# Optimization experiments

Measured on AMD Instinct MI355X. Metric: run time of the kernel, lower is better.

The kernel has to match this reference:

```python
import jax, jax.numpy as jnp
import numpy as np

N_NODES = 100000
N_EDGES = 1600000
IN_DIM = 128
OUT_DIM = 128


def setup_inputs() -> dict:
    key = jax.random.key(0)
    k1, k2, k3, k4, k5 = jax.random.split(key, 5)
    x = jax.random.normal(k1, (N_NODES, IN_DIM), dtype=jnp.float32)
    edge_index = jax.random.randint(k2, (2, N_EDGES), 0, N_NODES, dtype=jnp.int64)
    s = 1.0 / np.sqrt(IN_DIM)
    # PyG SAGEConv params: lin_l (neighbor branch, with bias), lin_r (root branch, no bias)
    W_l = jax.random.uniform(k3, (OUT_DIM, IN_DIM), jnp.float32, -s, s)
    b_l = jax.random.uniform(k4, (OUT_DIM,), jnp.float32, -s, s)
    W_r = jax.random.uniform(k5, (OUT_DIM, IN_DIM), jnp.float32, -s, s)
    return {"x": x, "edge_index": edge_index, "W_l": W_l, "b_l": b_l, "W_r": W_r}


def reference(x, edge_index, W_l, b_l, W_r):
    src = edge_index[0]  # message source j
    dst = edge_index[1]  # aggregation target i
    # mean aggregation of neighbor features at each target node
    msg_sum = jax.ops.segment_sum(x[src], dst, num_segments=N_NODES)  # [N, in]
    deg = jax.ops.segment_sum(jnp.ones((N_EDGES,), x.dtype), dst, num_segments=N_NODES)
    agg = msg_sum / jnp.maximum(deg, 1.0)[:, None]
    # out = lin_l(agg) + lin_r(x)
    out = agg @ W_l.T + b_l + x @ W_r.T  # [N, out]
    # L2 normalize (F.normalize, p=2, dim=-1, eps=1e-12)
    norm = jnp.sqrt(jnp.sum(out * out, axis=-1, keepdims=True))
    out = out / jnp.maximum(norm, 1e-12)
    return out
```

## Files before the change

kernel.cpp:

```cpp
#include <hip/hip_runtime.h>
#include <hip/hip_fp16.h>
#include <stdint.h>

#define NN 100000
#define D 128
#define W0 128
#define NB ((NN + W0 - 1) / W0)
#define C1 4096

typedef _Float16 f16x8 __attribute__((ext_vector_type(8)));
typedef float f32x4 __attribute__((ext_vector_type(4)));

static const size_t O_FLAG   = 0;
static const size_t O_BCNT   = 256;
static const size_t O_BSTART = O_BCNT + 4096;
static const size_t O_BCUR   = O_BSTART + 4096;
static const size_t O_WTL    = O_BCUR + 4096;
static const size_t O_WTR    = O_WTL + (size_t)D * D * 4;
static const size_t O_OFFS   = O_WTR + (size_t)D * D * 4;
static const size_t O_DEG    = O_OFFS + (size_t)(NN + 64) * 4;
static const size_t O_RECS   = O_DEG + (size_t)NN * 4;

__global__ void k_detect(const int* __restrict__ ei, int* flag, long long E) {
    int l = threadIdx.x;
    int bad = 0;
    if (l < E)       bad |= (ei[2 * l + 1] != 0);
    if (l + 64 < E)  bad |= (ei[2 * (l + 64) + 1] != 0);
    unsigned long long m = __ballot(bad);
    if (l == 0) *flag = (m == 0ull) ? 1 : 0;
}

__device__ __forceinline__ int edge_at(const int* ei, long long pos, int is64) {
    return is64 ? ei[2 * pos] : ei[pos];
}

__global__ void k_transpose(const float* __restrict__ Wl, const float* __restrict__ Wr,
                            float* __restrict__ WtL, float* __restrict__ WtR) {
    int t = blockIdx.x * 256 + threadIdx.x;
    if (t < D * D) {
        int o = t >> 7, k = t & 127;
        WtL[k * D + o] = Wl[t];
        WtR[k * D + o] = Wr[t];
    }
}

__global__ __launch_bounds__(256) void k_pack(const float* __restrict__ Wl,
                                              const float* __restrict__ Wr,
                                              __half* __restrict__ Bp) {
    int idx = blockIdx.x * 256 + threadIdx.x;
    if (idx >= 32768) return;
    int j  = idx & 7;
    int l  = (idx >> 3) & 63;
    int tt = (idx >> 9) & 7;
    int s  = idx >> 12;
    int col = tt * 16 + (l & 15);
    int k   = s * 32 + (l >> 4) * 8 + j;
    float v = (k < 128) ? Wl[col * 128 + k] : Wr[col * 128 + (k - 128)];
    Bp[idx] = __float2half_rn(v);
}

__global__ __launch_bounds__(256) void k_conv(const float* __restrict__ x,
                                              __half* __restrict__ xh, long long n4) {
    long long i = (long long)blockIdx.x * 256 + threadIdx.x;
    if (i >= n4) return;
    float4 v = ((const float4*)x)[i];
    __half2 h0 = __floats2half2_rn(v.x, v.y);
    __half2 h1 = __floats2half2_rn(v.z, v.w);
    ((__half2*)xh)[2 * i]     = h0;
    ((__half2*)xh)[2 * i + 1] = h1;
}

__global__ __launch_bounds__(256) void k_p1count(const int* __restrict__ ei,
                                                 const int* __restrict__ flag,
                                                 int* __restrict__ bcount,
                                                 int* __restrict__ bhist, long long E) {
    __shared__ int cnt[NB];
    for (int i = threadIdx.x; i < NB; i += 256) cnt[i] = 0;
    __syncthreads();
    int is64 = *flag;
    long long base = (long long)blockIdx.x * C1;
    for (int j = threadIdx.x; j < C1; j += 256) {
        long long e = base + j;
        if (e < E) {
            int d = edge_at(ei, E + e, is64);
            atomicAdd(&cnt[d >> 7], 1);
        }
    }
    __syncthreads();
    for (int i = threadIdx.x; i < NB; i += 256) {
        int c = cnt[i];
        if (bhist) bhist[(long long)blockIdx.x * NB + i] = c;
        if (c) atomicAdd(&bcount[i], c);
    }
}

__global__ __launch_bounds__(1024) void k_bscan(const int* __restrict__ bcount,
                                                int* __restrict__ bstart,
                                                int* __restrict__ bcur,
                                                int* __restrict__ offs) {
    __shared__ int sh[1024];
    int t = threadIdx.x;
    sh[t] = (t < NB) ? bcount[t] : 0;
    __syncthreads();
    for (int d = 1; d < 1024; d <<= 1) {
        int v = (t >= d) ? sh[t - d] : 0;
        __syncthreads();
        sh[t] += v;
        __syncthreads();
    }
    if (t < NB) {
        int ex = (t > 0) ? sh[t - 1] : 0;
        bstart[t] = ex;
        bcur[t] = ex;
    }
    if (t == NB - 1) {
        bstart[NB] = sh[NB - 1];
        offs[NN] = sh[NB - 1];
    }
}

__global__ __launch_bounds__(256) void k_p1scatter2(const int* __restrict__ ei,
                                                    const int* __restrict__ flag,
                                                    int* __restrict__ bcur,
                                                    const int* __restrict__ bhist,
                                                    unsigned int* __restrict__ recs,
                                                    long long E) {
    __shared__ int cnt[NB];
    __shared__ int rbase[NB];
    int t = threadIdx.x;
    const int* h = bhist + (long long)blockIdx.x * NB;
    for (int i = t; i < NB; i += 256) {
        int c = h[i];
        rbase[i] = c ? atomicAdd(&bcur[i], c) : 0;
        cnt[i] = 0;
    }
    __syncthreads();
    int is64 = *flag;
    long long base = (long long)blockIdx.x * C1;
    for (int j = t; j < C1; j += 256) {
        long long e = base + j;
        if (e < E) {
            int s = edge_at(ei, e, is64);
            int d = edge_at(ei, E + e, is64);
            int bu = d >> 7;
            int pos = rbase[bu] + atomicAdd(&cnt[bu], 1);
            recs[pos] = (unsigned)s | ((unsigned)(d & (W0 - 1)) << 20);
        }
    }
}

__global__ __launch_bounds__(256) void k_p1scatter(const int* __restrict__ ei,
                                                   const int* __restrict__ flag,
                                                   int* __restrict__ bcur,
                                                   unsigned int* __restrict__ recs,
                                                   long long E) {
    __shared__ int cnt[NB];
    __shared__ int rbase[NB];
    for (int i = threadIdx.x; i < NB; i += 256) cnt[i] = 0;
    __syncthreads();
    int is64 = *flag;
    long long base = (long long)blockIdx.x * C1;
    for (int j = threadIdx.x; j < C1; j += 256) {
        long long e = base + j;
        if (e < E) {
            int d = edge_at(ei, E + e, is64);
            atomicAdd(&cnt[d >> 7], 1);
        }
    }
    __syncthreads();
    for (int i = threadIdx.x; i < NB; i += 256) {
        int c = cnt[i];
        rbase[i] = c ? atomicAdd(&bcur[i], c) : 0;
    }
    __syncthreads();
    for (int i = threadIdx.x; i < NB; i += 256) cnt[i] = 0;
    __syncthreads();
    for (int j = threadIdx.x; j < C1; j += 256) {
        long long e = base + j;
        if (e < E) {
            int s = edge_at(ei, e, is64);
            int d = edge_at(ei, E + e, is64);
            int bu = d >> 7;
            int pos = rbase[bu] + atomicAdd(&cnt[bu], 1);
            recs[pos] = (unsigned)s | ((unsigned)(d & (W0 - 1)) << 20);
        }
    }
}

__global__ __launch_bounds__(256) void k_p2(const unsigned int* __restrict__ recs,
                                            const int* __restrict__ bstart,
                                            int* __restrict__ offs,
                                            int* __restrict__ srcs, int N) {
    __shared__ int cnt[W0];
    __shared__ int off[W0];
    int t = threadIdx.x;
    int bu = blockIdx.x;
    int e0 = bstart[bu], e1 = bstart[bu + 1];
    if (t < W0) cnt[t] = 0;
    __syncthreads();
    for (int e = e0 + t; e < e1; e += 256)
        atomicAdd(&cnt[recs[e] >> 20], 1);
    __syncthreads();
    if (t < W0) off[t] = cnt[t];
    __syncthreads();
    for (int d = 1; d < W0; d <<= 1) {
        int v = 0;
        if (t < W0 && t >= d) v = off[t - d];
        __syncthreads();
        if (t < W0) off[t] += v;
        __syncthreads();
    }
    if (t < W0) {
        int ex = (t > 0) ? off[t - 1] : 0;
        int node = bu * W0 + t;
        if (node < N) offs[node] = e0 + ex;
        cnt[t] = e0 + ex;
    }
    __syncthreads();
    for (int e = e0 + t; e < e1; e += 256) {
        unsigned r = recs[e];
        int pos = atomicAdd(&cnt[r >> 20], 1);
        srcs[pos] = (int)(r & 0xFFFFFu);
    }
}

__global__ __launch_bounds__(256) void k_agg_hh4(const __half* __restrict__ xh,
                                                 const int* __restrict__ offs,
                                                 const int* __restrict__ srcs,
                                                 __half* __restrict__ agg, int N) {
    int lane = threadIdx.x & 63;
    int wid  = __builtin_amdgcn_readfirstlane(threadIdx.x >> 6);
    int node = blockIdx.x * 4 + wid;
    if (node >= N) return;
    int e0 = offs[node], e1 = offs[node + 1];
    int grp = lane >> 4;
    int li  = lane & 15;
    float acc[8] = {0.f, 0.f, 0.f, 0.f, 0.f, 0.f, 0.f, 0.f};
    for (int e = e0; e < e1; e += 4) {
        int ee = e + grp;
        bool ok = ee < e1;
        int s = srcs[ok ? ee : e0];
        f16x8 v = *(const f16x8*)(xh + (long long)s * 128 + li * 8);
        if (ok) {
#pragma unroll
            for (int j = 0; j < 8; ++j) acc[j] += (float)v[j];
        }
    }
#pragma unroll
    for (int j = 0; j < 8; ++j) {
        acc[j] += __shfl_xor(acc[j], 16, 64);
        acc[j] += __shfl_xor(acc[j], 32, 64);
    }
    if (grp == 0) {
        float inv = 1.0f / fmaxf((float)(e1 - e0), 1.0f);
        __half2 o[4];
#pragma unroll
        for (int j = 0; j < 4; ++j)
            o[j] = __floats2half2_rn(acc[2 * j] * inv, acc[2 * j + 1] * inv);
        *(float4*)(agg + (long long)node * 128 + li * 8) = *(float4*)o;
    }
}

__global__ __launch_bounds__(256) void k_agg_h(const __half* __restrict__ xh,
                                               const int* __restrict__ offs,
                                               const int* __restrict__ srcs,
                                               float* agg, int N) {
    int lane = threadIdx.x & 63;
    int wid = __builtin_amdgcn_readfirstlane(threadIdx.x >> 6);
    int node = blockIdx.x * 4 + wid;
    if (node >= N) return;
    int e0 = offs[node], e1 = offs[node + 1];
    const __half2* x2 = (const __half2*)xh;
    float ax = 0.f, ay = 0.f;
    int e = e0;
    for (; e + 4 <= e1; e += 4) {
        int s0 = srcs[e], s1 = srcs[e + 1], s2 = srcs[e + 2], s3 = srcs[e + 3];
        float2 v0 = __half22float2(x2[(long long)s0 * 64 + lane]);
        float2 v1 = __half22float2(x2[(long long)s1 * 64 + lane]);
        float2 v2 = __half22float2(x2[(long long)s2 * 64 + lane]);
        float2 v3 = __half22float2(x2[(long long)s3 * 64 + lane]);
        ax += v0.x + v1.x + v2.x + v3.x;
        ay += v0.y + v1.y + v2.y + v3.y;
    }
    for (; e < e1; ++e) {
        int s = srcs[e];
        float2 v = __half22float2(x2[(long long)s * 64 + lane]);
        ax += v.x; ay += v.y;
    }
    float inv = 1.0f / fmaxf((float)(e1 - e0), 1.0f);
    float2 o; o.x = ax * inv; o.y = ay * inv;
    ((float2*)agg)[(long long)node * 64 + lane] = o;
}

__global__ __launch_bounds__(256) void k_agg(const float* __restrict__ x,
                                             const int* __restrict__ offs,
                                             const int* __restrict__ srcs,
                                             float* agg, int N) {
    int lane = threadIdx.x & 63;
    int wid = __builtin_amdgcn_readfirstlane(threadIdx.x >> 6);
    int node = blockIdx.x * 4 + wid;
    if (node >= N) return;
    int e0 = offs[node], e1 = offs[node + 1];
    const float2* x2 = (const float2*)x;
    float ax = 0.f, ay = 0.f;
    int e = e0;
    for (; e + 4 <= e1; e += 4) {
        int s0 = srcs[e], s1 = srcs[e + 1], s2 = srcs[e + 2], s3 = srcs[e + 3];
        float2 v0 = x2[(long long)s0 * 64 + lane];
        float2 v1 = x2[(long long)s1 * 64 + lane];
        float2 v2 = x2[(long long)s2 * 64 + lane];
        float2 v3 = x2[(long long)s3 * 64 + lane];
        ax += v0.x + v1.x + v2.x + v3.x;
        ay += v0.y + v1.y + v2.y + v3.y;
    }
    for (; e < e1; ++e) {
        int s = srcs[e];
        float2 v = x2[(long long)s * 64 + lane];
        ax += v.x; ay += v.y;
    }
    float inv = 1.0f / fmaxf((float)(e1 - e0), 1.0f);
    float2 o; o.x = ax * inv; o.y = ay * inv;
    ((float2*)agg)[(long long)node * 64 + lane] = o;
}

__global__ __launch_bounds__(256) void k_scatterB(const float* __restrict__ x,
                                                  const int* __restrict__ ei,
                                                  const int* __restrict__ flag,
                                                  float* out, float* deg, long long E) {
    int lane = threadIdx.x & 63;
    long long e = (long long)blockIdx.x * 4 + (threadIdx.x >> 6);
    if (e >= E) return;
    int is64 = *flag;
    int s = edge_at(ei, e, is64);
    int d = edge_at(ei, E + e, is64);
    atomicAdd(&out[(long long)d * D + lane], x[(long long)s * D + lane]);
    atomicAdd(&out[(long long)d * D + 64 + lane], x[(long long)s * D + 64 + lane]);
    if (lane == 0) atomicAdd(&deg[d], 1.0f);
}

__global__ void k_meanB(float* out, const float* __restrict__ deg) {
    long long i = (long long)blockIdx.x * 256 + threadIdx.x;
    if (i >= (long long)NN * D) return;
    out[i] *= 1.0f / fmaxf(deg[i >> 7], 1.0f);
}

__global__ __launch_bounds__(256) void k_gemm_m(const __half* __restrict__ aggh,
                                                const __half* __restrict__ xh,
                                                const __half* __restrict__ Bp,
                                                const float* __restrict__ bl,
                                                float* __restrict__ out, int N) {
    __shared__ __half Bs[32768];
    int t = threadIdx.x;
#pragma unroll
    for (int i = 0; i < 16; ++i) {
        int idx = t + i * 256;
        ((float4*)Bs)[idx] = ((const float4*)Bp)[idx];
    }
    int lane = t & 63;
    int wid  = t >> 6;
    int row0 = blockIdx.x * 128 + wid * 32;
    int rA = row0 + (lane & 15);
    int rB = rA + 16;
    long long ra = (rA < N) ? rA : (N - 1);
    long long rb = (rB < N) ? rB : (N - 1);
    int koff = (lane >> 4) * 8;

    f32x4 acc[2][8];
#pragma unroll
    for (int r = 0; r < 2; ++r)
#pragma unroll
        for (int c = 0; c < 8; ++c)
            acc[r][c] = (f32x4){0.f, 0.f, 0.f, 0.f};

    __syncthreads();

#pragma unroll
    for (int s = 0; s < 8; ++s) {
        const __half* Ap = (s < 4) ? aggh : xh;
        int kb = (s & 3) * 32 + koff;
        f16x8 a0 = *(const f16x8*)(Ap + ra * 128 + kb);
        f16x8 a1 = *(const f16x8*)(Ap + rb * 128 + kb);
        const __half* bs = Bs + s * 4096 + lane * 8;
#pragma unroll
        for (int tt = 0; tt < 8; ++tt) {
            f16x8 b = *(const f16x8*)(bs + tt * 512);
            acc[0][tt] = __builtin_amdgcn_mfma_f32_16x16x32_f16(a0, b, acc[0][tt], 0, 0, 0);
            acc[1][tt] = __builtin_amdgcn_mfma_f32_16x16x32_f16(a1, b, acc[1][tt], 0, 0, 0);
        }
    }

    float bias[8];
#pragma unroll
    for (int tt = 0; tt < 8; ++tt) bias[tt] = bl[tt * 16 + (lane & 15)];

#pragma unroll
    for (int rt = 0; rt < 2; ++rt) {
#pragma unroll
        for (int r = 0; r < 4; ++r) {
            int row = row0 + rt * 16 + (lane >> 4) * 4 + r;
            float v[8];
            float ss = 0.f;
#pragma unroll
            for (int tt = 0; tt < 8; ++tt) {
                v[tt] = acc[rt][tt][r] + bias[tt];
                ss = fmaf(v[tt], v[tt], ss);
            }
            ss += __shfl_xor(ss, 1, 64);
            ss += __shfl_xor(ss, 2, 64);
            ss += __shfl_xor(ss, 4, 64);
            ss += __shfl_xor(ss, 8, 64);
            float scale = 1.0f / fmaxf(sqrtf(ss), 1e-12f);
            if (row < N) {
                float* op = out + (long long)row * D + (lane & 15);
#pragma unroll
                for (int tt = 0; tt < 8; ++tt)
                    op[tt * 16] = v[tt] * scale;
            }
        }
    }
}

__global__ __launch_bounds__(256) void k_gemm(const float* __restrict__ x,
                                              const float* agg,
                                              const float* __restrict__ WtL,
                                              const float* __restrict__ WtR,
                                              const float* __restrict__ bl,
                                              float* out, int N) {
    __shared__ float Bs[64 * D];
    int t = threadIdx.x;
    int tx = t & 15;
    int ty = t >> 4;
    int row0 = blockIdx.x * 64 + ty * 4;
    int c0a = tx * 4;
    int c0b = 64 + tx * 4;

    float acc[4][8];
    float4 b0 = *(const float4*)(bl + c0a);
    float4 b1 = *(const float4*)(bl + c0b);
#pragma unroll
    for (int r = 0; r < 4; ++r) {
        acc[r][0] = b0.x; acc[r][1] = b0.y; acc[r][2] = b0.z; acc[r][3] = b0.w;
        acc[r][4] = b1.x; acc[r][5] = b1.y; acc[r][6] = b1.z; acc[r][7] = b1.w;
    }

    long long rws[4];
#pragma unroll
    for (int r = 0; r < 4; ++r) {
        int rr = row0 + r;
        rws[r] = (rr < N) ? (long long)rr : (long long)(N - 1);
    }

    for (int phase = 0; phase < 2; ++phase) {
        const float* A = phase ? x : agg;
        const float* W = phase ? WtR : WtL;
        const float4* Ar0 = (const float4*)(A + rws[0] * D);
        const float4* Ar1 = (const float4*)(A + rws[1] * D);
        const float4* Ar2 = (const float4*)(A + rws[2] * D);
        const float4* Ar3 = (const float4*)(A + rws[3] * D);

        for (int half = 0; half < 2; ++half) {
            if (phase | half) __syncthreads();
#pragma unroll
            for (int i = 0; i < 8; ++i) {
                int idx = t + i * 256;
                ((float4*)Bs)[idx] = ((const float4*)(W + half * 64 * D))[idx];
            }
            __syncthreads();

#pragma unroll 2
            for (int k4 = 0; k4 < 16; ++k4) {
                int ak4 = half * 16 + k4;
                float4 av[4];
                av[0] = Ar0[ak4]; av[1] = Ar1[ak4]; av[2] = Ar2[ak4]; av[3] = Ar3[ak4];
#pragma unroll
                for (int kk = 0; kk < 4; ++kk) {
                    int k = k4 * 4 + kk;
                    float4 w0 = *(const float4*)&Bs[k * D + c0a];
                    float4 w1 = *(const float4*)&Bs[k * D + c0b];
#pragma unroll
                    for (int r = 0; r < 4; ++r) {
                        float a = (kk == 0) ? av[r].x : (kk == 1) ? av[r].y
                                 : (kk == 2) ? av[r].z : av[r].w;
                        acc[r][0] = fmaf(a, w0.x, acc[r][0]);
                        acc[r][1] = fmaf(a, w0.y, acc[r][1]);
                        acc[r][2] = fmaf(a, w0.z, acc[r][2]);
                        acc[r][3] = fmaf(a, w0.w, acc[r][3]);
                        acc[r][4] = fmaf(a, w1.x, acc[r][4]);
                        acc[r][5] = fmaf(a, w1.y, acc[r][5]);
                        acc[r][6] = fmaf(a, w1.z, acc[r][6]);
                        acc[r][7] = fmaf(a, w1.w, acc[r][7]);
                    }
                }
            }
        }
    }

#pragma unroll
    for (int r = 0; r < 4; ++r) {
        float s = 0.f;
#pragma unroll
        for (int j = 0; j < 8; ++j) s = fmaf(acc[r][j], acc[r][j], s);
        s += __shfl_xor(s, 1, 64);
        s += __shfl_xor(s, 2, 64);
        s += __shfl_xor(s, 4, 64);
        s += __shfl_xor(s, 8, 64);
        float scale = 1.0f / fmaxf(sqrtf(s), 1e-12f);
        int rr = row0 + r;
        if (rr < N) {
            float4 v0, v1;
            v0.x = acc[r][0] * scale; v0.y = acc[r][1] * scale;
            v0.z = acc[r][2] * scale; v0.w = acc[r][3] * scale;
            v1.x = acc[r][4] * scale; v1.y = acc[r][5] * scale;
            v1.z = acc[r][6] * scale; v1.w = acc[r][7] * scale;
            float* op = out + (long long)rr * D;
            *(float4*)(op + c0a) = v0;
            *(float4*)(op + c0b) = v1;
        }
    }
}

extern "C" void kernel_launch(void* const* d_in, const int* in_sizes, int n_in,
                              void* d_out, int out_size, void* d_ws, size_t ws_size,
                              hipStream_t stream) {
    const float* x  = (const float*)d_in[0];
    const int*   ei = (const int*)d_in[1];
    const float* Wl = (const float*)d_in[2];
    const float* bl = (const float*)d_in[3];
    const float* Wr = (const float*)d_in[4];
    float* out = (float*)d_out;
    const long long E = (long long)in_sizes[1] / 2;

    char* ws = (char*)d_ws;
    int*      flag   = (int*)(ws + O_FLAG);
    int*      bcount = (int*)(ws + O_BCNT);
    int*      bstart = (int*)(ws + O_BSTART);
    int*      bcur   = (int*)(ws + O_BCUR);
    float*    WtL    = (float*)(ws + O_WTL);
    float*    WtR    = (float*)(ws + O_WTR);
    __half*   Bph    = (__half*)(ws + O_WTL);
    int*      offs   = (int*)(ws + O_OFFS);
    float*    deg    = (float*)(ws + O_DEG);
    unsigned* recs   = (unsigned*)(ws + O_RECS);
    int*      srcs   = (int*)(ws + O_RECS + (size_t)E * 4);
    const size_t O_XH = O_RECS + (size_t)E * 8;
    __half*   xh     = (__half*)(ws + O_XH);
    const size_t O_AGGH = O_XH + (size_t)NN * D * 2;
    __half*   aggh   = (__half*)(ws + O_AGGH);
    const size_t O_BHIST = O_AGGH + (size_t)NN * D * 2;
    int*      bhist  = (int*)(ws + O_BHIST);

    int pblocks = (int)((E + C1 - 1) / C1);
    size_t planA_bytes  = O_RECS + (size_t)E * 8;
    size_t fp16_bytes   = O_XH + (size_t)NN * D * 2;
    size_t mfma_bytes   = O_AGGH + (size_t)NN * D * 2;
    size_t merged_bytes = O_BHIST + (size_t)pblocks * NB * 4;
    bool planA    = ws_size >= planA_bytes;
    bool useH     = ws_size >= fp16_bytes;
    bool useM     = planA && (ws_size >= mfma_bytes);
    bool useMerge = useM && (ws_size >= merged_bytes);

    k_detect<<<1, 64, 0, stream>>>(ei, flag, E);
    if (useM)
        k_pack<<<128, 256, 0, stream>>>(Wl, Wr, Bph);
    else
        k_transpose<<<(D * D + 255) / 256, 256, 0, stream>>>(Wl, Wr, WtL, WtR);

    if (planA) {
        hipMemsetAsync(ws + O_BCNT, 0, (size_t)NB * 4, stream);
        if (useH) {
            long long n4 = (long long)NN * D / 4;
            k_conv<<<(int)((n4 + 255) / 256), 256, 0, stream>>>(x, xh, n4);
        }
        k_p1count<<<pblocks, 256, 0, stream>>>(ei, flag, bcount,
                                               useMerge ? bhist : (int*)nullptr, E);
        k_bscan<<<1, 1024, 0, stream>>>(bcount, bstart, bcur, offs);
        if (useMerge)
            k_p1scatter2<<<pblocks, 256, 0, stream>>>(ei, flag, bcur, bhist, recs, E);
        else
            k_p1scatter<<<pblocks, 256, 0, stream>>>(ei, flag, bcur, recs, E);
        k_p2<<<NB, 256, 0, stream>>>(recs, bstart, offs, srcs, NN);
        if (useM) {
            k_agg_hh4<<<(NN + 3) / 4, 256, 0, stream>>>(xh, offs, srcs, aggh, NN);
            k_gemm_m<<<(NN + 127) / 128, 256, 0, stream>>>(aggh, xh, Bph, bl, out, NN);
            return;
        }
        if (useH)
            k_agg_h<<<(NN + 3) / 4, 256, 0, stream>>>(xh, offs, srcs, out, NN);
        else
            k_agg<<<(NN + 3) / 4, 256, 0, stream>>>(x, offs, srcs, out, NN);
    } else {
        hipMemsetAsync(out, 0, (size_t)NN * D * 4, stream);
        hipMemsetAsync(ws + O_DEG, 0, (size_t)NN * 4, stream);
        k_scatterB<<<(int)((E + 3) / 4), 256, 0, stream>>>(x, ei, flag, out, deg, E);
        k_meanB<<<(int)(((long long)NN * D + 255) / 256), 256, 0, stream>>>(out, deg);
    }
    k_gemm<<<(NN + 63) / 64, 256, 0, stream>>>(x, out, WtL, WtR, bl, out, NN);
}
```

Measured before the change: 266.7 us.

## Split aggregation across feature slices with per-block node chunks

Replaces the one-wave-per-node fp16 gather with a kernel where each block handles one 16-column feature slice for a 256-node chunk. Eight blocks cover the eight slices. Within a wave, 4 nodes × 8 edges × 2 halves are processed at once, and partial sums are reduced by shuffles. The intent is to narrow the working set touched per block so the gathered rows get better cache locality. In exchange each source row is fetched in 32-byte pieces by eight separate blocks and the srcs/offs reads are repeated eight times.

```diff
diff --git a/kernel.cpp b/kernel.cpp
--- a/kernel.cpp
+++ b/kernel.cpp
@@ -224,40 +224,47 @@
     }
 }
 
-__global__ __launch_bounds__(256) void k_agg_hh4(const __half* __restrict__ xh,
-                                                 const int* __restrict__ offs,
-                                                 const int* __restrict__ srcs,
-                                                 __half* __restrict__ agg, int N) {
-    int lane = threadIdx.x & 63;
-    int wid  = __builtin_amdgcn_readfirstlane(threadIdx.x >> 6);
-    int node = blockIdx.x * 4 + wid;
-    if (node >= N) return;
-    int e0 = offs[node], e1 = offs[node + 1];
-    int grp = lane >> 4;
-    int li  = lane & 15;
-    float acc[8] = {0.f, 0.f, 0.f, 0.f, 0.f, 0.f, 0.f, 0.f};
-    for (int e = e0; e < e1; e += 4) {
-        int ee = e + grp;
-        bool ok = ee < e1;
-        int s = srcs[ok ? ee : e0];
-        f16x8 v = *(const f16x8*)(xh + (long long)s * 128 + li * 8);
-        if (ok) {
-#pragma unroll
-            for (int j = 0; j < 8; ++j) acc[j] += (float)v[j];
-        }
-    }
-#pragma unroll
-    for (int j = 0; j < 8; ++j) {
-        acc[j] += __shfl_xor(acc[j], 16, 64);
-        acc[j] += __shfl_xor(acc[j], 32, 64);
-    }
-    if (grp == 0) {
-        float inv = 1.0f / fmaxf((float)(e1 - e0), 1.0f);
-        __half2 o[4];
-#pragma unroll
-        for (int j = 0; j < 4; ++j)
-            o[j] = __floats2half2_rn(acc[2 * j] * inv, acc[2 * j + 1] * inv);
-        *(float4*)(agg + (long long)node * 128 + li * 8) = *(float4*)o;
+__global__ __launch_bounds__(256) void k_agg_s(const __half* __restrict__ xh,
+                                               const int* __restrict__ offs,
+                                               const int* __restrict__ srcs,
+                                               __half* __restrict__ agg, int N) {
+    int slice = blockIdx.x & 7;
+    int chunk = blockIdx.x >> 3;
+    int lane  = threadIdx.x & 63;
+    int wid   = __builtin_amdgcn_readfirstlane(threadIdx.x >> 6);
+    int n_in  = lane >> 4;
+    int e_in  = (lane >> 1) & 7;
+    int h     = lane & 1;
+    int dbase = slice * 16 + h * 8;
+
+    for (int r = 0; r < 16; ++r) {
+        int node = chunk * 256 + r * 16 + wid * 4 + n_in;
+        if (node >= N) return;
+        int e0 = offs[node], e1 = offs[node + 1];
+        float acc[8] = {0.f, 0.f, 0.f, 0.f, 0.f, 0.f, 0.f, 0.f};
+        for (int e = e0; e < e1; e += 8) {
+            int ee = e + e_in;
+            if (ee < e1) {
+                int s = srcs[ee];
+                f16x8 v = *(const f16x8*)(xh + (long long)s * 128 + dbase);
+#pragma unroll
+                for (int j = 0; j < 8; ++j) acc[j] += (float)v[j];
+            }
+        }
+#pragma unroll
+        for (int j = 0; j < 8; ++j) {
+            acc[j] += __shfl_xor(acc[j], 2, 64);
+            acc[j] += __shfl_xor(acc[j], 4, 64);
+            acc[j] += __shfl_xor(acc[j], 8, 64);
+        }
+        if (e_in == 0) {
+            float inv = 1.0f / fmaxf((float)(e1 - e0), 1.0f);
+            __half2 o[4];
+#pragma unroll
+            for (int j = 0; j < 4; ++j)
+                o[j] = __floats2half2_rn(acc[2 * j] * inv, acc[2 * j + 1] * inv);
+            *(float4*)(agg + (long long)node * 128 + dbase) = *(float4*)o;
+        }
     }
 }
 
@@ -580,7 +587,8 @@
             k_p1scatter<<<pblocks, 256, 0, stream>>>(ei, flag, bcur, recs, E);
         k_p2<<<NB, 256, 0, stream>>>(recs, bstart, offs, srcs, NN);
         if (useM) {
-            k_agg_hh4<<<(NN + 3) / 4, 256, 0, stream>>>(xh, offs, srcs, aggh, NN);
+            int nchunk = (NN + 255) / 256;
+            k_agg_s<<<8 * nchunk, 256, 0, stream>>>(xh, offs, srcs, aggh, NN);
             k_gemm_m<<<(NN + 127) / 128, 256, 0, stream>>>(aggh, xh, Bph, bl, out, NN);
             return;
         }
```

Result: slower. 387.7 us (+45.4%).

## Fuse CSR preprocessing into one cooperative kernel with grid syncs

Applied to the files above, without the earlier changes.

Replaces the chain of detect, pack, convert, count, scan, scatter and per-bucket sort kernels with a single cooperative kernel of NB blocks that uses grid.sync between phases, removing several launches and the memset. Each block now loops over multiple edge chunks and keeps its histogram in shared memory across the grid barrier, so the per-chunk global bhist buffer is no longer needed. The aggregation kernel is swapped back to a half2-per-lane variant with 8-way unrolled gathers. Risks include cooperative-launch occupancy limits for 782 blocks with large shared arrays, fewer blocks doing the edge pass, and grid-barrier cost.

```diff
diff --git a/kernel.cpp b/kernel.cpp
--- a/kernel.cpp
+++ b/kernel.cpp
@@ -1,6 +1,9 @@
 #include <hip/hip_runtime.h>
 #include <hip/hip_fp16.h>
+#include <hip/hip_cooperative_groups.h>
 #include <stdint.h>
+
+namespace cg = cooperative_groups;
 
 #define NN 100000
 #define D 128
@@ -21,6 +24,273 @@
 static const size_t O_DEG    = O_OFFS + (size_t)(NN + 64) * 4;
 static const size_t O_RECS   = O_DEG + (size_t)NN * 4;
 
+__device__ __forceinline__ int edge_at(const int* ei, long long pos, int is64) {
+    return is64 ? ei[2 * pos] : ei[pos];
+}
+
+__global__ __launch_bounds__(256) void k_fused(
+        const float* __restrict__ x, const int* __restrict__ ei,
+        const float* __restrict__ Wl, const float* __restrict__ Wr,
+        __half* __restrict__ xh, __half* __restrict__ Bp,
+        int* __restrict__ bcount, int* __restrict__ bstart,
+        int* __restrict__ bcur, int* __restrict__ offs,
+        unsigned int* __restrict__ recs, int* __restrict__ srcs,
+        long long E, int pblocks)
+{
+    cg::grid_group grid = cg::this_grid();
+    __shared__ int cnt[NB];
+    __shared__ int rbase[NB];
+    __shared__ int ssum[256];
+    __shared__ int s_is64;
+    int t = threadIdx.x;
+    int b = blockIdx.x;
+
+    if (t < 64) {
+        int bad = 0;
+        if (t < E)      bad |= (ei[2 * t + 1] != 0);
+        if (t + 64 < E) bad |= (ei[2 * (t + 64) + 1] != 0);
+        unsigned long long m = __ballot(bad);
+        if (t == 0) s_is64 = (m == 0ull) ? 1 : 0;
+    }
+    for (int i = t; i < NB; i += 256) cnt[i] = 0;
+    if (b == 0) for (int i = t; i < NB; i += 256) bcount[i] = 0;
+    __syncthreads();
+    int is64 = s_is64;
+
+    const long long n4 = (long long)NN * D / 4;
+    for (long long i = (long long)b * 256 + t; i < n4; i += (long long)NB * 256) {
+        float4 v = ((const float4*)x)[i];
+        ((__half2*)xh)[2 * i]     = __floats2half2_rn(v.x, v.y);
+        ((__half2*)xh)[2 * i + 1] = __floats2half2_rn(v.z, v.w);
+    }
+    {
+        int idx = b * 256 + t;
+        if (idx < 32768) {
+            int j  = idx & 7;
+            int l  = (idx >> 3) & 63;
+            int tt = (idx >> 9) & 7;
+            int s  = idx >> 12;
+            int col = tt * 16 + (l & 15);
+            int k   = s * 32 + (l >> 4) * 8 + j;
+            float v = (k < 128) ? Wl[col * 128 + k] : Wr[col * 128 + (k - 128)];
+            Bp[idx] = __float2half_rn(v);
+        }
+    }
+    for (int chunk = b; chunk < pblocks; chunk += NB) {
+        long long base = (long long)chunk * C1;
+        for (int j = t; j < C1; j += 256) {
+            long long e = base + j;
+            if (e < E) atomicAdd(&cnt[edge_at(ei, E + e, is64) >> 7], 1);
+        }
+    }
+    grid.sync();
+
+    for (int i = t; i < NB; i += 256) {
+        int c = cnt[i];
+        if (c) atomicAdd(&bcount[i], c);
+    }
+    grid.sync();
+
+    if (b == 0) {
+        int vals[4];
+        int mysum = 0;
+#pragma unroll
+        for (int k = 0; k < 4; ++k) {
+            int i = t * 4 + k;
+            int v = (i < NB) ? bcount[i] : 0;
+            vals[k] = mysum;
+            mysum += v;
+        }
+        ssum[t] = mysum;
+        __syncthreads();
+        for (int d = 1; d < 256; d <<= 1) {
+            int v = (t >= d) ? ssum[t - d] : 0;
+            __syncthreads();
+            ssum[t] += v;
+            __syncthreads();
+        }
+        int base0 = (t > 0) ? ssum[t - 1] : 0;
+#pragma unroll
+        for (int k = 0; k < 4; ++k) {
+            int i = t * 4 + k;
+            if (i < NB) {
+                int ex = base0 + vals[k];
+                bstart[i] = ex;
+                bcur[i] = ex;
+            }
+        }
+        if (t == 255) { bstart[NB] = ssum[255]; offs[NN] = ssum[255]; }
+    }
+    grid.sync();
+
+    for (int i = t; i < NB; i += 256) {
+        int c = cnt[i];
+        rbase[i] = c ? atomicAdd(&bcur[i], c) : 0;
+        cnt[i] = 0;
+    }
+    __syncthreads();
+    for (int chunk = b; chunk < pblocks; chunk += NB) {
+        long long base = (long long)chunk * C1;
+        for (int j = t; j < C1; j += 256) {
+            long long e = base + j;
+            if (e < E) {
+                int s = edge_at(ei, e, is64);
+                int d = edge_at(ei, E + e, is64);
+                int bu = d >> 7;
+                int pos = rbase[bu] + atomicAdd(&cnt[bu], 1);
+                recs[pos] = (unsigned)s | ((unsigned)(d & (W0 - 1)) << 20);
+            }
+        }
+    }
+    grid.sync();
+
+    {
+        int e0 = bstart[b], e1 = bstart[b + 1];
+        if (t < W0) cnt[t] = 0;
+        __syncthreads();
+        for (int e = e0 + t; e < e1; e += 256)
+            atomicAdd(&cnt[recs[e] >> 20], 1);
+        __syncthreads();
+        if (t < W0) rbase[t] = cnt[t];
+        __syncthreads();
+        for (int d = 1; d < W0; d <<= 1) {
+            int v = 0;
+            if (t < W0 && t >= d) v = rbase[t - d];
+            __syncthreads();
+            if (t < W0) rbase[t] += v;
+            __syncthreads();
+        }
+        if (t < W0) {
+            int ex = (t > 0) ? rbase[t - 1] : 0;
+            int node = b * W0 + t;
+            if (node < NN) offs[node] = e0 + ex;
+            cnt[t] = e0 + ex;
+        }
+        __syncthreads();
+        for (int e = e0 + t; e < e1; e += 256) {
+            unsigned r = recs[e];
+            int pos = atomicAdd(&cnt[r >> 20], 1);
+            srcs[pos] = (int)(r & 0xFFFFFu);
+        }
+    }
+}
+
+__global__ __launch_bounds__(256) void k_agg_hh(const __half* __restrict__ xh,
+                                                const int* __restrict__ offs,
+                                                const int* __restrict__ srcs,
+                                                __half* __restrict__ agg, int N) {
+    int lane = threadIdx.x & 63;
+    int wid  = __builtin_amdgcn_readfirstlane(threadIdx.x >> 6);
+    int node = blockIdx.x * 4 + wid;
+    if (node >= N) return;
+    int e0 = offs[node], e1 = offs[node + 1];
+    const __half2* x2 = (const __half2*)xh;
+    float ax = 0.f, ay = 0.f;
+    int e = e0;
+    for (; e + 8 <= e1; e += 8) {
+        int ss[8];
+#pragma unroll
+        for (int u = 0; u < 8; ++u) ss[u] = srcs[e + u];
+        __half2 h[8];
+#pragma unroll
+        for (int u = 0; u < 8; ++u) h[u] = x2[(long long)ss[u] * 64 + lane];
+#pragma unroll
+        for (int u = 0; u < 8; ++u) {
+            float2 v = __half22float2(h[u]);
+            ax += v.x; ay += v.y;
+        }
+    }
+    for (; e + 2 <= e1; e += 2) {
+        int s0 = srcs[e], s1 = srcs[e + 1];
+        float2 v0 = __half22float2(x2[(long long)s0 * 64 + lane]);
+        float2 v1 = __half22float2(x2[(long long)s1 * 64 + lane]);
+        ax += v0.x + v1.x;
+        ay += v0.y + v1.y;
+    }
+    if (e < e1) {
+        float2 v = __half22float2(x2[(long long)srcs[e] * 64 + lane]);
+        ax += v.x; ay += v.y;
+    }
+    float inv = 1.0f / fmaxf((float)(e1 - e0), 1.0f);
+    ((__half2*)agg)[(long long)node * 64 + lane] = __floats2half2_rn(ax * inv, ay * inv);
+}
+
+__global__ __launch_bounds__(256) void k_gemm_m(const __half* __restrict__ aggh,
+                                                const __half* __restrict__ xh,
+                                                const __half* __restrict__ Bp,
+                                                const float* __restrict__ bl,
+                                                float* __restrict__ out, int N) {
+    __shared__ __half Bs[32768];
+    int t = threadIdx.x;
+#pragma unroll
+    for (int i = 0; i < 16; ++i) {
+        int idx = t + i * 256;
+        ((float4*)Bs)[idx] = ((const float4*)Bp)[idx];
+    }
+    int lane = t & 63;
+    int wid  = t >> 6;
+    int row0 = blockIdx.x * 128 + wid * 32;
+    int rA = row0 + (lane & 15);
+    int rB = rA + 16;
+    long long ra = (rA < N) ? rA : (N - 1);
+    long long rb = (rB < N) ? rB : (N - 1);
+    int koff = (lane >> 4) * 8;
+
+    f32x4 acc[2][8];
+#pragma unroll
+    for (int r = 0; r < 2; ++r)
+#pragma unroll
+        for (int c = 0; c < 8; ++c)
+            acc[r][c] = (f32x4){0.f, 0.f, 0.f, 0.f};
+
+    __syncthreads();
+
+#pragma unroll
+    for (int s = 0; s < 8; ++s) {
+        const __half* Ap = (s < 4) ? aggh : xh;
+        int kb = (s & 3) * 32 + koff;
+        f16x8 a0 = *(const f16x8*)(Ap + ra * 128 + kb);
+        f16x8 a1 = *(const f16x8*)(Ap + rb * 128 + kb);
+        const __half* bs = Bs + s * 4096 + lane * 8;
+#pragma unroll
+        for (int tt = 0; tt < 8; ++tt) {
+            f16x8 b = *(const f16x8*)(bs + tt * 512);
+            acc[0][tt] = __builtin_amdgcn_mfma_f32_16x16x32_f16(a0, b, acc[0][tt], 0, 0, 0);
+            acc[1][tt] = __builtin_amdgcn_mfma_f32_16x16x32_f16(a1, b, acc[1][tt], 0, 0, 0);
+        }
+    }
+
+    float bias[8];
+#pragma unroll
+    for (int tt = 0; tt < 8; ++tt) bias[tt] = bl[tt * 16 + (lane & 15)];
+
+#pragma unroll
+    for (int rt = 0; rt < 2; ++rt) {
+#pragma unroll
+        for (int r = 0; r < 4; ++r) {
+            int row = row0 + rt * 16 + (lane >> 4) * 4 + r;
+            float v[8];
+            float ss = 0.f;
+#pragma unroll
+            for (int tt = 0; tt < 8; ++tt) {
+                v[tt] = acc[rt][tt][r] + bias[tt];
+                ss = fmaf(v[tt], v[tt], ss);
+            }
+            ss += __shfl_xor(ss, 1, 64);
+            ss += __shfl_xor(ss, 2, 64);
+            ss += __shfl_xor(ss, 4, 64);
+            ss += __shfl_xor(ss, 8, 64);
+            float scale = 1.0f / fmaxf(sqrtf(ss), 1e-12f);
+            if (row < N) {
+                float* op = out + (long long)row * D + (lane & 15);
+#pragma unroll
+                for (int tt = 0; tt < 8; ++tt)
+                    op[tt * 16] = v[tt] * scale;
+            }
+        }
+    }
+}
+
 __global__ void k_detect(const int* __restrict__ ei, int* flag, long long E) {
     int l = threadIdx.x;
     int bad = 0;
@@ -30,10 +300,6 @@
     if (l == 0) *flag = (m == 0ull) ? 1 : 0;
 }
 
-__device__ __forceinline__ int edge_at(const int* ei, long long pos, int is64) {
-    return is64 ? ei[2 * pos] : ei[pos];
-}
-
 __global__ void k_transpose(const float* __restrict__ Wl, const float* __restrict__ Wr,
                             float* __restrict__ WtL, float* __restrict__ WtR) {
     int t = blockIdx.x * 256 + threadIdx.x;
@@ -44,36 +310,9 @@
     }
 }
 
-__global__ __launch_bounds__(256) void k_pack(const float* __restrict__ Wl,
-                                              const float* __restrict__ Wr,
-                                              __half* __restrict__ Bp) {
-    int idx = blockIdx.x * 256 + threadIdx.x;
-    if (idx >= 32768) return;
-    int j  = idx & 7;
-    int l  = (idx >> 3) & 63;
-    int tt = (idx >> 9) & 7;
-    int s  = idx >> 12;
-    int col = tt * 16 + (l & 15);
-    int k   = s * 32 + (l >> 4) * 8 + j;
-    float v = (k < 128) ? Wl[col * 128 + k] : Wr[col * 128 + (k - 128)];
-    Bp[idx] = __float2half_rn(v);
-}
-
-__global__ __launch_bounds__(256) void k_conv(const float* __restrict__ x,
-                                              __half* __restrict__ xh, long long n4) {
-    long long i = (long long)blockIdx.x * 256 + threadIdx.x;
-    if (i >= n4) return;
-    float4 v = ((const float4*)x)[i];
-    __half2 h0 = __floats2half2_rn(v.x, v.y);
-    __half2 h1 = __floats2half2_rn(v.z, v.w);
-    ((__half2*)xh)[2 * i]     = h0;
-    ((__half2*)xh)[2 * i + 1] = h1;
-}
-
 __global__ __launch_bounds__(256) void k_p1count(const int* __restrict__ ei,
                                                  const int* __restrict__ flag,
-                                                 int* __restrict__ bcount,
-                                                 int* __restrict__ bhist, long long E) {
+                                                 int* __restrict__ bcount, long long E) {
     __shared__ int cnt[NB];
     for (int i = threadIdx.x; i < NB; i += 256) cnt[i] = 0;
     __syncthreads();
@@ -81,15 +320,11 @@
     long long base = (long long)blockIdx.x * C1;
     for (int j = threadIdx.x; j < C1; j += 256) {
         long long e = base + j;
-        if (e < E) {
-            int d = edge_at(ei, E + e, is64);
-            atomicAdd(&cnt[d >> 7], 1);
-        }
+        if (e < E) atomicAdd(&cnt[edge_at(ei, E + e, is64) >> 7], 1);
     }
     __syncthreads();
     for (int i = threadIdx.x; i < NB; i += 256) {
         int c = cnt[i];
-        if (bhist) bhist[(long long)blockIdx.x * NB + i] = c;
         if (c) atomicAdd(&bcount[i], c);
     }
 }
@@ -116,36 +351,6 @@
     if (t == NB - 1) {
         bstart[NB] = sh[NB - 1];
         offs[NN] = sh[NB - 1];
-    }
-}
-
-__global__ __launch_bounds__(256) void k_p1scatter2(const int* __restrict__ ei,
-                                                    const int* __restrict__ flag,
-                                                    int* __restrict__ bcur,
-                                                    const int* __restrict__ bhist,
-                                                    unsigned int* __restrict__ recs,
-                                                    long long E) {
-    __shared__ int cnt[NB];
-    __shared__ int rbase[NB];
-    int t = threadIdx.x;
-    const int* h = bhist + (long long)blockIdx.x * NB;
-    for (int i = t; i < NB; i += 256) {
-        int c = h[i];
-        rbase[i] = c ? atomicAdd(&bcur[i], c) : 0;
-        cnt[i] = 0;
-    }
-    __syncthreads();
-    int is64 = *flag;
-    long long base = (long long)blockIdx.x * C1;
-    for (int j = t; j < C1; j += 256) {
-        long long e = base + j;
-        if (e < E) {
-            int s = edge_at(ei, e, is64);
-            int d = edge_at(ei, E + e, is64);
-            int bu = d >> 7;
-            int pos = rbase[bu] + atomicAdd(&cnt[bu], 1);
-            recs[pos] = (unsigned)s | ((unsigned)(d & (W0 - 1)) << 20);
-        }
     }
 }
 
@@ -162,10 +367,7 @@
     long long base = (long long)blockIdx.x * C1;
     for (int j = threadIdx.x; j < C1; j += 256) {
         long long e = base + j;
-        if (e < E) {
-            int d = edge_at(ei, E + e, is64);
-            atomicAdd(&cnt[d >> 7], 1);
-        }
+        if (e < E) atomicAdd(&cnt[edge_at(ei, E + e, is64) >> 7], 1);
     }
     __syncthreads();
     for (int i = threadIdx.x; i < NB; i += 256) {
@@ -224,72 +426,13 @@
     }
 }
 
-__global__ __launch_bounds__(256) void k_agg_hh4(const __half* __restrict__ xh,
-                                                 const int* __restrict__ offs,
-                                                 const int* __restrict__ srcs,
-                                                 __half* __restrict__ agg, int N) {
-    int lane = threadIdx.x & 63;
-    int wid  = __builtin_amdgcn_readfirstlane(threadIdx.x >> 6);
-    int node = blockIdx.x * 4 + wid;
-    if (node >= N) return;
-    int e0 = offs[node], e1 = offs[node + 1];
-    int grp = lane >> 4;
-    int li  = lane & 15;
-    float acc[8] = {0.f, 0.f, 0.f, 0.f, 0.f, 0.f, 0.f, 0.f};
-    for (int e = e0; e < e1; e += 4) {
-        int ee = e + grp;
-        bool ok = ee < e1;
-        int s = srcs[ok ? ee : e0];
-        f16x8 v = *(const f16x8*)(xh + (long long)s * 128 + li * 8);
-        if (ok) {
-#pragma unroll
-            for (int j = 0; j < 8; ++j) acc[j] += (float)v[j];
-        }
-    }
-#pragma unroll
-    for (int j = 0; j < 8; ++j) {
-        acc[j] += __shfl_xor(acc[j], 16, 64);
-        acc[j] += __shfl_xor(acc[j], 32, 64);
-    }
-    if (grp == 0) {
-        float inv = 1.0f / fmaxf((float)(e1 - e0), 1.0f);
-        __half2 o[4];
-#pragma unroll
-        for (int j = 0; j < 4; ++j)
-            o[j] = __floats2half2_rn(acc[2 * j] * inv, acc[2 * j + 1] * inv);
-        *(float4*)(agg + (long long)node * 128 + li * 8) = *(float4*)o;
-    }
-}
-
-__global__ __launch_bounds__(256) void k_agg_h(const __half* __restrict__ xh,
-                                               const int* __restrict__ offs,
-                                               const int* __restrict__ srcs,
-                                               float* agg, int N) {
-    int lane = threadIdx.x & 63;
-    int wid = __builtin_amdgcn_readfirstlane(threadIdx.x >> 6);
-    int node = blockIdx.x * 4 + wid;
-    if (node >= N) return;
-    int e0 = offs[node], e1 = offs[node + 1];
-    const __half2* x2 = (const __half2*)xh;
-    float ax = 0.f, ay = 0.f;
-    int e = e0;
-    for (; e + 4 <= e1; e += 4) {
-        int s0 = srcs[e], s1 = srcs[e + 1], s2 = srcs[e + 2], s3 = srcs[e + 3];
-        float2 v0 = __half22float2(x2[(long long)s0 * 64 + lane]);
-        float2 v1 = __half22float2(x2[(long long)s1 * 64 + lane]);
-        float2 v2 = __half22float2(x2[(long long)s2 * 64 + lane]);
-        float2 v3 = __half22float2(x2[(long long)s3 * 64 + lane]);
-        ax += v0.x + v1.x + v2.x + v3.x;
-        ay += v0.y + v1.y + v2.y + v3.y;
-    }
-    for (; e < e1; ++e) {
-        int s = srcs[e];
-        float2 v = __half22float2(x2[(long long)s * 64 + lane]);
-        ax += v.x; ay += v.y;
-    }
-    float inv = 1.0f / fmaxf((float)(e1 - e0), 1.0f);
-    float2 o; o.x = ax * inv; o.y = ay * inv;
-    ((float2*)agg)[(long long)node * 64 + lane] = o;
+__global__ __launch_bounds__(256) void k_conv(const float* __restrict__ x,
+                                              __half* __restrict__ xh, long long n4) {
+    long long i = (long long)blockIdx.x * 256 + threadIdx.x;
+    if (i >= n4) return;
+    float4 v = ((const float4*)x)[i];
+    ((__half2*)xh)[2 * i]     = __floats2half2_rn(v.x, v.y);
+    ((__half2*)xh)[2 * i + 1] = __floats2half2_rn(v.z, v.w);
 }
 
 __global__ __launch_bounds__(256) void k_agg(const float* __restrict__ x,
@@ -344,82 +487,6 @@
     out[i] *= 1.0f / fmaxf(deg[i >> 7], 1.0f);
 }
 
-__global__ __launch_bounds__(256) void k_gemm_m(const __half* __restrict__ aggh,
-                                                const __half* __restrict__ xh,
-                                                const __half* __restrict__ Bp,
-                                                const float* __restrict__ bl,
-                                                float* __restrict__ out, int N) {
-    __shared__ __half Bs[32768];
-    int t = threadIdx.x;
-#pragma unroll
-    for (int i = 0; i < 16; ++i) {
-        int idx = t + i * 256;
-        ((float4*)Bs)[idx] = ((const float4*)Bp)[idx];
-    }
-    int lane = t & 63;
-    int wid  = t >> 6;
-    int row0 = blockIdx.x * 128 + wid * 32;
-    int rA = row0 + (lane & 15);
-    int rB = rA + 16;
-    long long ra = (rA < N) ? rA : (N - 1);
-    long long rb = (rB < N) ? rB : (N - 1);
-    int koff = (lane >> 4) * 8;
-
-    f32x4 acc[2][8];
-#pragma unroll
-    for (int r = 0; r < 2; ++r)
-#pragma unroll
-        for (int c = 0; c < 8; ++c)
-            acc[r][c] = (f32x4){0.f, 0.f, 0.f, 0.f};
-
-    __syncthreads();
-
-#pragma unroll
-    for (int s = 0; s < 8; ++s) {
-        const __half* Ap = (s < 4) ? aggh : xh;
-        int kb = (s & 3) * 32 + koff;
-        f16x8 a0 = *(const f16x8*)(Ap + ra * 128 + kb);
-        f16x8 a1 = *(const f16x8*)(Ap + rb * 128 + kb);
-        const __half* bs = Bs + s * 4096 + lane * 8;
-#pragma unroll
-        for (int tt = 0; tt < 8; ++tt) {
-            f16x8 b = *(const f16x8*)(bs + tt * 512);
-            acc[0][tt] = __builtin_amdgcn_mfma_f32_16x16x32_f16(a0, b, acc[0][tt], 0, 0, 0);
-            acc[1][tt] = __builtin_amdgcn_mfma_f32_16x16x32_f16(a1, b, acc[1][tt], 0, 0, 0);
-        }
-    }
-
-    float bias[8];
-#pragma unroll
-    for (int tt = 0; tt < 8; ++tt) bias[tt] = bl[tt * 16 + (lane & 15)];
-
-#pragma unroll
-    for (int rt = 0; rt < 2; ++rt) {
-#pragma unroll
-        for (int r = 0; r < 4; ++r) {
-            int row = row0 + rt * 16 + (lane >> 4) * 4 + r;
-            float v[8];
-            float ss = 0.f;
-#pragma unroll
-            for (int tt = 0; tt < 8; ++tt) {
-                v[tt] = acc[rt][tt][r] + bias[tt];
-                ss = fmaf(v[tt], v[tt], ss);
-            }
-            ss += __shfl_xor(ss, 1, 64);
-            ss += __shfl_xor(ss, 2, 64);
-            ss += __shfl_xor(ss, 4, 64);
-            ss += __shfl_xor(ss, 8, 64);
-            float scale = 1.0f / fmaxf(sqrtf(ss), 1e-12f);
-            if (row < N) {
-                float* op = out + (long long)row * D + (lane & 15);
-#pragma unroll
-                for (int tt = 0; tt < 8; ++tt)
-                    op[tt * 16] = v[tt] * scale;
-            }
-        }
-    }
-}
-
 __global__ __launch_bounds__(256) void k_gemm(const float* __restrict__ x,
                                               const float* agg,
                                               const float* __restrict__ WtL,
@@ -546,48 +613,41 @@
     __half*   xh     = (__half*)(ws + O_XH);
     const size_t O_AGGH = O_XH + (size_t)NN * D * 2;
     __half*   aggh   = (__half*)(ws + O_AGGH);
-    const size_t O_BHIST = O_AGGH + (size_t)NN * D * 2;
-    int*      bhist  = (int*)(ws + O_BHIST);
 
     int pblocks = (int)((E + C1 - 1) / C1);
-    size_t planA_bytes  = O_RECS + (size_t)E * 8;
-    size_t fp16_bytes   = O_XH + (size_t)NN * D * 2;
-    size_t mfma_bytes   = O_AGGH + (size_t)NN * D * 2;
-    size_t merged_bytes = O_BHIST + (size_t)pblocks * NB * 4;
-    bool planA    = ws_size >= planA_bytes;
-    bool useH     = ws_size >= fp16_bytes;
-    bool useM     = planA && (ws_size >= mfma_bytes);
-    bool useMerge = useM && (ws_size >= merged_bytes);
+    size_t planA_bytes = O_RECS + (size_t)E * 8;
+    size_t fp16_bytes  = O_XH + (size_t)NN * D * 2;
+    size_t mfma_bytes  = O_AGGH + (size_t)NN * D * 2;
+    bool planA = ws_size >= planA_bytes;
+    bool useH  = ws_size >= fp16_bytes;
+    bool useM  = planA && (ws_size >= mfma_bytes);
+
+    if (useM) {
+        long long E_ = E;
+        int pb_ = pblocks;
+        void* kargs[] = {
+            (void*)&x, (void*)&ei, (void*)&Wl, (void*)&Wr,
+            (void*)&xh, (void*)&Bph,
+            (void*)&bcount, (void*)&bstart, (void*)&bcur, (void*)&offs,
+            (void*)&recs, (void*)&srcs, (void*)&E_, (void*)&pb_
+        };
+        hipLaunchCooperativeKernel((const void*)k_fused, dim3(NB), dim3(256),
+                                   kargs, 0, stream);
+        k_agg_hh<<<(NN + 3) / 4, 256, 0, stream>>>(xh, offs, srcs, aggh, NN);
+        k_gemm_m<<<(NN + 127) / 128, 256, 0, stream>>>(aggh, xh, Bph, bl, out, NN);
+        return;
+    }
 
     k_detect<<<1, 64, 0, stream>>>(ei, flag, E);
-    if (useM)
-        k_pack<<<128, 256, 0, stream>>>(Wl, Wr, Bph);
-    else
-        k_transpose<<<(D * D + 255) / 256, 256, 0, stream>>>(Wl, Wr, WtL, WtR);
+    k_transpose<<<(D * D + 255) / 256, 256, 0, stream>>>(Wl, Wr, WtL, WtR);
 
     if (planA) {
         hipMemsetAsync(ws + O_BCNT, 0, (size_t)NB * 4, stream);
-        if (useH) {
-            long long n4 = (long long)NN * D / 4;
-            k_conv<<<(int)((n4 + 255) / 256), 256, 0, stream>>>(x, xh, n4);
-        }
-        k_p1count<<<pblocks, 256, 0, stream>>>(ei, flag, bcount,
-                                               useMerge ? bhist : (int*)nullptr, E);
+        k_p1count<<<pblocks, 256, 0, stream>>>(ei, flag, bcount, E);
         k_bscan<<<1, 1024, 0, stream>>>(bcount, bstart, bcur, offs);
-        if (useMerge)
-            k_p1scatter2<<<pblocks, 256, 0, stream>>>(ei, flag, bcur, bhist, recs, E);
-        else
-            k_p1scatter<<<pblocks, 256, 0, stream>>>(ei, flag, bcur, recs, E);
+        k_p1scatter<<<pblocks, 256, 0, stream>>>(ei, flag, bcur, recs, E);
         k_p2<<<NB, 256, 0, stream>>>(recs, bstart, offs, srcs, NN);
-        if (useM) {
-            k_agg_hh4<<<(NN + 3) / 4, 256, 0, stream>>>(xh, offs, srcs, aggh, NN);
-            k_gemm_m<<<(NN + 127) / 128, 256, 0, stream>>>(aggh, xh, Bph, bl, out, NN);
-            return;
-        }
-        if (useH)
-            k_agg_h<<<(NN + 3) / 4, 256, 0, stream>>>(xh, offs, srcs, out, NN);
-        else
-            k_agg<<<(NN + 3) / 4, 256, 0, stream>>>(x, offs, srcs, out, NN);
+        k_agg<<<(NN + 3) / 4, 256, 0, stream>>>(x, offs, srcs, out, NN);
     } else {
         hipMemsetAsync(out, 0, (size_t)NN * D * 4, stream);
         hipMemsetAsync(ws + O_DEG, 0, (size_t)NN * 4, stream);
```

Measured after the change: 598.7 us. 124% more time.
